# Performance work log

Hardware: AMD Instinct MI355X
Metric: run time of the kernel (lower is better)

Reference implementation:

```python
import jax, jax.numpy as jnp
import numpy as np

# structural constants (from dg config / init_kwargs)
B = 8192      # batch (L=1)
N = 64        # number of columns
C = 16        # one-hot width per column
D = N * C     # 1024
NUM = 32      # first NUM columns are numeric (use info['range'])
NCAUSAL = 16  # causal_cols = range(16)
K = 8         # info['range'][i] is [C, K]
HS = 1024
HP = 1024
TAU = 0.7
SMOOTH = 0.1  # kwargs['smoothing']


def setup_inputs() -> dict:
    key = jax.random.key(0)
    ks = jax.random.split(key, 20)
    s = 0.02
    inp = {
        'x': jax.random.uniform(ks[0], (B, D), dtype=jnp.float32),
        'truth_x': jax.random.normal(ks[1], (B, N), dtype=jnp.float32),
        # selector: Linear(D,HS) -> ReLU -> Linear(HS,N) -> Sigmoid
        'sel_w1': jax.random.normal(ks[2], (D, HS)) * s,
        'sel_b1': jnp.zeros((HS,), jnp.float32),
        'sel_w2': jax.random.normal(ks[3], (HS, N)) * s,
        'sel_b2': jnp.zeros((N,), jnp.float32),
        # perturber: D->HP->HP->HP->D with ReLU between
        'pw1': jax.random.normal(ks[4], (D, HP)) * s,
        'pb1': jnp.zeros((HP,), jnp.float32),
        'pw2': jax.random.normal(ks[5], (HP, HP)) * s,
        'pb2': jnp.zeros((HP,), jnp.float32),
        'pw3': jax.random.normal(ks[6], (HP, HP)) * s,
        'pb3': jnp.zeros((HP,), jnp.float32),
        'pw4': jax.random.normal(ks[7], (HP, D)) * s,
        'pb4': jnp.zeros((D,), jnp.float32),
        # dg.info['range'][i] for numeric columns: [NUM, C, K]
        'ranges': jax.random.normal(ks[8], (NUM, C, K), dtype=jnp.float32),
        # pre-drawn noise (training branch)
        'unif_a': jax.random.uniform(ks[9], (B, N), minval=1e-6, maxval=1.0 - 1e-6),
        'unif_b': jax.random.uniform(ks[10], (B, N), minval=1e-6, maxval=1.0 - 1e-6),
        'gumbel': jax.random.gumbel(ks[11], (B, N, C), dtype=jnp.float32),
    }
    return inp


def reference(x, truth_x, sel_w1, sel_b1, sel_w2, sel_b2,
              pw1, pb1, pw2, pb2, pw3, pb3, pw4, pb4,
              ranges, unif_a, unif_b, gumbel):
    # selector -> P in (0,1), shape [B, N]
    P = jax.nn.sigmoid(jax.nn.relu(x @ sel_w1 + sel_b1) @ sel_w2 + sel_b2)
    # relaxed Bernoulli (Sample_Bernoulli, training branch)
    ga = -jnp.log(-jnp.log(unif_a))
    gb = -jnp.log(-jnp.log(unif_b))
    no_logits = P * jnp.exp(ga) / TAU
    de_logits = no_logits + (1.0 - P) * jnp.exp(gb) / TAU
    probs = no_logits / de_logits                       # [B, N]
    # perturber MLP -> W, shape [B, D]
    h = jax.nn.relu(x @ pw1 + pb1)
    h = jax.nn.relu(h @ pw2 + pb2)
    h = jax.nn.relu(h @ pw3 + pb3)
    W = h @ pw4 + pb4
    # per-column blocks
    xr = x.reshape(B, N, C)
    logits = W.reshape(B, N, C)
    # data-dependent causal masking for causal columns
    curr = jnp.argmax(xr, axis=-1)                      # [B, N]
    causal = (jnp.arange(N) < NCAUSAL)[None, :, None]   # [1, N, 1]
    below = jnp.arange(C)[None, None, :] < curr[:, :, None]
    mask = jnp.where(causal & below, -100.0, jnp.where(causal, 1.0, 0.0))
    logits = logits + mask
    # label smoothing then Gumbel-softmax (soft), per Sample_Categorical
    pr = jax.nn.softmax(logits, axis=-1)
    pr = (1.0 - SMOOTH) * pr + SMOOTH / C
    logits = jnp.log(pr)
    y = jax.nn.softmax((logits + gumbel) / TAU, axis=-1)  # [B, N, C]
    # numeric columns: map categorical sample through range table, mix with truth
    xt_num = jnp.einsum('bnc,nck->bnk', y[:, :NUM], ranges).mean(axis=-1)  # [B, NUM]
    p_num = probs[:, :NUM]
    out_num = p_num * xt_num + (1.0 - p_num) * truth_x[:, :NUM]           # [B, NUM]
    # categorical columns: mix relaxed sample with original one-hot block
    p_cat = probs[:, NUM:, None]
    out_cat = p_cat * y[:, NUM:] + (1.0 - p_cat) * xr[:, NUM:]            # [B, N-NUM, C]
    xcf = jnp.concatenate([out_num, out_cat.reshape(B, (N - NUM) * C)], axis=1)
    return truth_x, xcf, P, W
```

## Files before the change

kernel.cpp:

```cpp
#include <hip/hip_runtime.h>
#include <hip/hip_bf16.h>
#include <cstdint>

#define B_DIM 8192
#define N_DIM 64
#define C_DIM 16
#define D_DIM 1024
#define NUM 32
#define NCAUSAL 16
#define K_RANGES 8
#define HS 1024
#define HP 1024
#define TAU 0.7f
#define SMOOTH 0.1f

typedef __bf16 bf16x8 __attribute__((ext_vector_type(8)));
typedef float f32x16 __attribute__((ext_vector_type(16)));

typedef const __attribute__((address_space(1))) uint32_t* gas_ptr;
typedef __attribute__((address_space(3))) uint32_t* las_ptr;

__device__ __forceinline__ void gld_lds16(const void* g, void* l) {
    __builtin_amdgcn_global_load_lds((gas_ptr)(uintptr_t)g,
                                     (las_ptr)(uint32_t)(uintptr_t)l,
                                     16, 0, 0);
}

__device__ __forceinline__ int swz(int r) { return (r & 3) ^ ((r >> 2) & 3); }

template <int ACT>
__device__ __forceinline__ void gemm_body8(
    const ushort* __restrict__ Ag, const ushort* __restrict__ Bg,
    const float* __restrict__ bias,
    float* __restrict__ Cf, __hip_bfloat16* __restrict__ Cb,
    int lda, int Nout, int ldC, int K, long m0, long n0,
    uint4 (*As)[512], uint4 (*Bs)[512])
{
    const int tid  = threadIdx.x;
    const int wave = tid >> 6;
    const int ln31 = tid & 31, blk = (tid >> 5) & 1;
    const int wr = wave >> 2, wc = wave & 3;

    const int row = tid >> 2;
    const int ch  = (tid & 3) ^ swz(row);
    const ushort* aSrc = Ag + (m0 + row) * (long)lda + ch * 8;
    const ushort* bSrc = Bg + (n0 + row) * (long)K   + ch * 8;
    const int ldsOff = wave << 6;

    f32x16 acc[2];
    acc[0] = (f32x16)(0.0f);
    acc[1] = (f32x16)(0.0f);

#define ISSUE_STAGE8(buf, kt)                                                  \
    {                                                                          \
        gld_lds16(aSrc + (kt), &As[buf][ldsOff]);                              \
        gld_lds16(bSrc + (kt), &Bs[buf][ldsOff]);                              \
    }

    const int nt = K >> 5;
    ISSUE_STAGE8(0, 0);
    ISSUE_STAGE8(1, 32);

    int rb = 0;
    for (int t = 0; t < nt; ++t) {
        if (t < nt - 1) {
            asm volatile("s_waitcnt vmcnt(2)" ::: "memory");
        } else {
            asm volatile("s_waitcnt vmcnt(0)" ::: "memory");
        }
        __builtin_amdgcn_s_barrier();

        if (t + 2 < nt) {
            int sb = rb + 2; if (sb >= 3) sb -= 3;
            ISSUE_STAGE8(sb, (t + 2) * 32);
        }

        bf16x8 af[2][2], bfr[2];
#pragma unroll
        for (int ks = 0; ks < 2; ++ks) {
            int c = ks * 2 + blk;
#pragma unroll
            for (int mi = 0; mi < 2; ++mi) {
                int r = wr * 64 + mi * 32 + ln31;
                af[ks][mi] = __builtin_bit_cast(bf16x8, As[rb][r * 4 + (c ^ swz(r))]);
            }
            int n = wc * 32 + ln31;
            bfr[ks] = __builtin_bit_cast(bf16x8, Bs[rb][n * 4 + (c ^ swz(n))]);
        }
#pragma unroll
        for (int ks = 0; ks < 2; ++ks)
#pragma unroll
            for (int mi = 0; mi < 2; ++mi)
                acc[mi] = __builtin_amdgcn_mfma_f32_32x32x16_bf16(
                    af[ks][mi], bfr[ks], acc[mi], 0, 0, 0);

        rb = (rb == 2) ? 0 : rb + 1;
    }
#undef ISSUE_STAGE8

    long col = n0 + wc * 32 + ln31;
    if (col < Nout) {
        float bs = bias ? bias[col] : 0.0f;
#pragma unroll
        for (int mi = 0; mi < 2; ++mi) {
#pragma unroll
            for (int reg = 0; reg < 16; ++reg) {
                long r2 = m0 + wr * 64 + mi * 32 + (reg & 3) + 8 * (reg >> 2) + 4 * blk;
                float v = acc[mi][reg] + bs;
                if (ACT == 1) {
                    v = fmaxf(v, 0.0f);
                    Cb[r2 * (long)ldC + col] = __float2bfloat16(v);
                } else if (ACT == 2) {
                    v = 1.0f / (1.0f + __expf(-v));
                    Cf[r2 * (long)ldC + col] = v;
                } else {
                    Cf[r2 * (long)ldC + col] = v;
                }
            }
        }
    }
}

__device__ __forceinline__ void xcd_remap(int& bx, int& by)
{
    int gx  = gridDim.x;
    int nwg = gx * gridDim.y;
    int lin = by * gx + bx;
    int cpx = nwg >> 3;
    int sw  = (lin & 7) * cpx + (lin >> 3);
    by = sw / gx;
    bx = sw - by * gx;
}

template <int ACT>
__global__ __launch_bounds__(512, 4) void gemm8(
    const __hip_bfloat16* __restrict__ A, const __hip_bfloat16* __restrict__ Bt,
    const float* __restrict__ bias,
    float* __restrict__ Cf, __hip_bfloat16* __restrict__ Cb,
    int lda, int Nout, int ldC, int K)
{
    __shared__ uint4 As[3][512];
    __shared__ uint4 Bs[3][512];
    int bx = blockIdx.x, by = blockIdx.y;
    xcd_remap(bx, by);
    gemm_body8<ACT>((const ushort*)A, (const ushort*)Bt, bias, Cf, Cb,
                    lda, Nout, ldC, K,
                    (long)by * 128, (long)bx * 128, As, Bs);
}

__global__ __launch_bounds__(512, 4) void gemm8_fused23(
    const __hip_bfloat16* __restrict__ act1,
    const __hip_bfloat16* __restrict__ p2t, const float* __restrict__ pb2,
    __hip_bfloat16* __restrict__ actB,
    const __hip_bfloat16* __restrict__ w2t, const float* __restrict__ sel_b2,
    float* __restrict__ outP)
{
    __shared__ uint4 As[3][512];
    __shared__ uint4 Bs[3][512];
    int bx = blockIdx.x, by = blockIdx.y;
    xcd_remap(bx, by);
    long m0 = (long)by * 128;
    if (bx < 8) {
        gemm_body8<1>((const ushort*)(act1 + 1024), (const ushort*)p2t, pb2,
                      nullptr, actB, 2048, 1024, 1024, 1024,
                      m0, (long)bx * 128, As, Bs);
    } else {
        gemm_body8<2>((const ushort*)act1, (const ushort*)w2t, sel_b2,
                      outP, nullptr, 2048, 64, 64, 1024,
                      m0, 0, As, Bs);
    }
}

struct PrepArgs {
    const float* src[6];
    __hip_bfloat16* dst[6];
    int Nsrc[6];
    int Npad[6];
    const float* ranges; float* rmean;
    const float* b1; const float* b2; float* bcat;
    const float* x; __hip_bfloat16* xbf;
};

__global__ void prep_kernel(PrepArgs a)
{
    int z = blockIdx.z;
    int tx = threadIdx.x, ty = threadIdx.y;
    int t = ty * 32 + tx;
    if (z == 7) {
        int bid = blockIdx.y * 32 + blockIdx.x;
        const float4* s4 = (const float4*)a.x;
        for (int i = bid * 256 + t; i < B_DIM * D_DIM / 4; i += 1024 * 256) {
            float4 v = s4[i];
            __hip_bfloat16* d = a.xbf + (size_t)i * 4;
            d[0] = __float2bfloat16(v.x);
            d[1] = __float2bfloat16(v.y);
            d[2] = __float2bfloat16(v.z);
            d[3] = __float2bfloat16(v.w);
        }
        return;
    }
    if (z == 6) {
        if (blockIdx.x || blockIdx.y) return;
        for (int j = t; j < NUM * C_DIM; j += 256) {
            float s = 0.0f;
#pragma unroll
            for (int k = 0; k < K_RANGES; ++k) s += a.ranges[j * K_RANGES + k];
            a.rmean[j] = s * (1.0f / K_RANGES);
        }
        for (int j = t; j < 1024; j += 256) {
            a.bcat[j]        = a.b1[j];
            a.bcat[1024 + j] = a.b2[j];
        }
        return;
    }
    const int Nsrc = a.Nsrc[z], Npad = a.Npad[z];
    int n0 = blockIdx.x * 32, k0 = blockIdx.y * 32;
    if (n0 >= Npad) return;
    const float* src = a.src[z];
    __hip_bfloat16* dst = a.dst[z];
    __shared__ float tile[32][33];
#pragma unroll
    for (int i = 0; i < 32; i += 8) {
        int k = k0 + ty + i, n = n0 + tx;
        tile[ty + i][tx] = (n < Nsrc) ? src[(size_t)k * Nsrc + n] : 0.0f;
    }
    __syncthreads();
#pragma unroll
    for (int i = 0; i < 32; i += 8) {
        int n = n0 + ty + i, k = k0 + tx;
        dst[(size_t)n * D_DIM + k] = __float2bfloat16(tile[tx][ty + i]);
    }
}

__global__ void finalize_kernel(
    const float* __restrict__ x, const float* __restrict__ truth,
    const float* __restrict__ ua, const float* __restrict__ ub,
    const float* __restrict__ gum, const float* __restrict__ rmean,
    const float* __restrict__ P, const float* __restrict__ W,
    float* __restrict__ out_truth, float* __restrict__ out_xcf)
{
    int idx = blockIdx.x * 256 + threadIdx.x;
    if (idx >= B_DIM * N_DIM) return;
    int b = idx >> 6, n = idx & 63;

    float tx = truth[idx];
    out_truth[idx] = tx;

    float p  = P[idx];
    float ea = -1.0f / logf(ua[idx]);
    float eb = -1.0f / logf(ub[idx]);
    float no = p * ea;
    float probs = no / (no + (1.0f - p) * eb);

    const float* Wrow = W + (size_t)idx * 16;
    const float* grow = gum + (size_t)idx * 16;
    float lo[16], g[16], xv[16];
#pragma unroll
    for (int c = 0; c < 16; c += 4) {
        float4 v = *(const float4*)(Wrow + c);
        lo[c] = v.x; lo[c + 1] = v.y; lo[c + 2] = v.z; lo[c + 3] = v.w;
        float4 gv = *(const float4*)(grow + c);
        g[c] = gv.x; g[c + 1] = gv.y; g[c + 2] = gv.z; g[c + 3] = gv.w;
    }

    bool needx = (n < NCAUSAL) || (n >= NUM);
    if (needx) {
        const float* xrow = x + (size_t)idx * 16;
#pragma unroll
        for (int c = 0; c < 16; c += 4) {
            float4 v = *(const float4*)(xrow + c);
            xv[c] = v.x; xv[c + 1] = v.y; xv[c + 2] = v.z; xv[c + 3] = v.w;
        }
    }

    if (n < NCAUSAL) {
        int curr = 0; float best = xv[0];
#pragma unroll
        for (int c = 1; c < 16; ++c)
            if (xv[c] > best) { best = xv[c]; curr = c; }
#pragma unroll
        for (int c = 0; c < 16; ++c) lo[c] += (c < curr) ? -100.0f : 1.0f;
    }

    float mx = lo[0];
#pragma unroll
    for (int c = 1; c < 16; ++c) mx = fmaxf(mx, lo[c]);
    float s = 0.0f, pr[16];
#pragma unroll
    for (int c = 0; c < 16; ++c) { pr[c] = __expf(lo[c] - mx); s += pr[c]; }
    float inv = 1.0f / s;
#pragma unroll
    for (int c = 0; c < 16; ++c)
        pr[c] = (1.0f - SMOOTH) * pr[c] * inv + (SMOOTH / C_DIM);

    float t[16];
    float mx2 = -1e30f;
#pragma unroll
    for (int c = 0; c < 16; ++c) {
        t[c] = (__logf(pr[c]) + g[c]) * (1.0f / TAU);
        mx2 = fmaxf(mx2, t[c]);
    }
    float s2 = 0.0f;
#pragma unroll
    for (int c = 0; c < 16; ++c) { t[c] = __expf(t[c] - mx2); s2 += t[c]; }
    float inv2 = 1.0f / s2;

    if (n < NUM) {
        float xt = 0.0f;
#pragma unroll
        for (int c = 0; c < 16; ++c) xt += t[c] * inv2 * rmean[n * 16 + c];
        out_xcf[(size_t)b * 544 + n] = probs * xt + (1.0f - probs) * tx;
    } else {
        float* o = out_xcf + (size_t)b * 544 + 32 + (size_t)(n - NUM) * 16;
#pragma unroll
        for (int c = 0; c < 16; ++c)
            o[c] = probs * t[c] * inv2 + (1.0f - probs) * xv[c];
    }
}

extern "C" void kernel_launch(void* const* d_in, const int* in_sizes, int n_in,
                              void* d_out, int out_size, void* d_ws, size_t ws_size,
                              hipStream_t stream)
{
    const float* x      = (const float*)d_in[0];
    const float* truth  = (const float*)d_in[1];
    const float* sel_w1 = (const float*)d_in[2];
    const float* sel_b1 = (const float*)d_in[3];
    const float* sel_w2 = (const float*)d_in[4];
    const float* sel_b2 = (const float*)d_in[5];
    const float* pw1    = (const float*)d_in[6];
    const float* pb1    = (const float*)d_in[7];
    const float* pw2    = (const float*)d_in[8];
    const float* pb2    = (const float*)d_in[9];
    const float* pw3    = (const float*)d_in[10];
    const float* pb3    = (const float*)d_in[11];
    const float* pw4    = (const float*)d_in[12];
    const float* pb4    = (const float*)d_in[13];
    const float* ranges = (const float*)d_in[14];
    const float* ua     = (const float*)d_in[15];
    const float* ub     = (const float*)d_in[16];
    const float* gum    = (const float*)d_in[17];

    float* out       = (float*)d_out;
    float* out_truth = out;
    float* out_xcf   = out + 524288;
    float* out_P     = out + 4980736;
    float* out_W     = out + 5505024;

    char* w = (char*)d_ws;
    size_t off = 0;
    __hip_bfloat16* A0   = (__hip_bfloat16*)(w + off); off += (size_t)B_DIM * D_DIM * 2;
    __hip_bfloat16* act1 = (__hip_bfloat16*)(w + off); off += (size_t)B_DIM * 2048 * 2;
    __hip_bfloat16* actB = (__hip_bfloat16*)(w + off); off += (size_t)B_DIM * HP * 2;
    __hip_bfloat16* actC = (__hip_bfloat16*)(w + off); off += (size_t)B_DIM * HP * 2;
    __hip_bfloat16* Wcat = (__hip_bfloat16*)(w + off); off += (size_t)2048 * D_DIM * 2;
    __hip_bfloat16* w2t  = (__hip_bfloat16*)(w + off); off += (size_t)128 * HS * 2;
    __hip_bfloat16* p2t  = (__hip_bfloat16*)(w + off); off += (size_t)HP * HP * 2;
    __hip_bfloat16* p3t  = (__hip_bfloat16*)(w + off); off += (size_t)HP * HP * 2;
    __hip_bfloat16* p4t  = (__hip_bfloat16*)(w + off); off += (size_t)D_DIM * HP * 2;
    float* rmean         = (float*)(w + off);          off += 512 * 4;
    float* bcat          = (float*)(w + off);          off += 2048 * 4;
    if (ws_size < off) return;

    PrepArgs pa;
    pa.src[0] = sel_w1; pa.dst[0] = Wcat;               pa.Nsrc[0] = HS;    pa.Npad[0] = 1024;
    pa.src[1] = pw1;    pa.dst[1] = Wcat + 1024 * 1024; pa.Nsrc[1] = HP;    pa.Npad[1] = 1024;
    pa.src[2] = sel_w2; pa.dst[2] = w2t;                pa.Nsrc[2] = N_DIM; pa.Npad[2] = 128;
    pa.src[3] = pw2;    pa.dst[3] = p2t;                pa.Nsrc[3] = HP;    pa.Npad[3] = 1024;
    pa.src[4] = pw3;    pa.dst[4] = p3t;                pa.Nsrc[4] = HP;    pa.Npad[4] = 1024;
    pa.src[5] = pw4;    pa.dst[5] = p4t;                pa.Nsrc[5] = D_DIM; pa.Npad[5] = 1024;
    pa.ranges = ranges; pa.rmean = rmean;
    pa.b1 = sel_b1; pa.b2 = pb1; pa.bcat = bcat;
    pa.x = x; pa.xbf = A0;

    prep_kernel<<<dim3(32, 32, 8), dim3(32, 8), 0, stream>>>(pa);

    gemm8<1><<<dim3(16, 64), 512, 0, stream>>>(A0, Wcat, bcat, nullptr, act1,
                                               D_DIM, 2048, 2048, D_DIM);
    gemm8_fused23<<<dim3(9, 64), 512, 0, stream>>>(act1, p2t, pb2, actB, w2t,
                                                   sel_b2, out_P);
    gemm8<1><<<dim3(8, 64), 512, 0, stream>>>(actB, p3t, pb3, nullptr, actC,
                                              HP, HP, HP, HP);
    gemm8<0><<<dim3(8, 64), 512, 0, stream>>>(actC, p4t, pb4, out_W, nullptr,
                                              HP, D_DIM, D_DIM, HP);

    finalize_kernel<<<(B_DIM * N_DIM + 255) / 256, 256, 0, stream>>>(
        x, truth, ua, ub, gum, rmean, out_P, out_W, out_truth, out_xcf);
}
```

Before: 293.7 us.

## Restructure bf16 GEMMs into intra-block split-K with LDS reduction

Replaces the 3-stage pipelined GEMM body with a split-K design. Each of two wave groups handles half of a 64-wide K slice with a 64x64 per-wave sub-tile, and the partial accumulators are reduced through LDS before the bias/activation epilogue. The goal is more reuse of register fragments per MFMA (2x2 outputs per wave instead of 2x1) and fewer barriers per K. The cost is double buffering instead of triple, an extra LDS reduction pass, and higher register use (4 accumulators) that may hurt occupancy under launch_bounds(512,4).

Result: slower. 309.3 us (+5.3%).

```diff
diff --git a/kernel.cpp b/kernel.cpp
--- a/kernel.cpp
+++ b/kernel.cpp
@@ -28,99 +28,6 @@
 
 __device__ __forceinline__ int swz(int r) { return (r & 3) ^ ((r >> 2) & 3); }
 
-template <int ACT>
-__device__ __forceinline__ void gemm_body8(
-    const ushort* __restrict__ Ag, const ushort* __restrict__ Bg,
-    const float* __restrict__ bias,
-    float* __restrict__ Cf, __hip_bfloat16* __restrict__ Cb,
-    int lda, int Nout, int ldC, int K, long m0, long n0,
-    uint4 (*As)[512], uint4 (*Bs)[512])
-{
-    const int tid  = threadIdx.x;
-    const int wave = tid >> 6;
-    const int ln31 = tid & 31, blk = (tid >> 5) & 1;
-    const int wr = wave >> 2, wc = wave & 3;
-
-    const int row = tid >> 2;
-    const int ch  = (tid & 3) ^ swz(row);
-    const ushort* aSrc = Ag + (m0 + row) * (long)lda + ch * 8;
-    const ushort* bSrc = Bg + (n0 + row) * (long)K   + ch * 8;
-    const int ldsOff = wave << 6;
-
-    f32x16 acc[2];
-    acc[0] = (f32x16)(0.0f);
-    acc[1] = (f32x16)(0.0f);
-
-#define ISSUE_STAGE8(buf, kt)                                                  \
-    {                                                                          \
-        gld_lds16(aSrc + (kt), &As[buf][ldsOff]);                              \
-        gld_lds16(bSrc + (kt), &Bs[buf][ldsOff]);                              \
-    }
-
-    const int nt = K >> 5;
-    ISSUE_STAGE8(0, 0);
-    ISSUE_STAGE8(1, 32);
-
-    int rb = 0;
-    for (int t = 0; t < nt; ++t) {
-        if (t < nt - 1) {
-            asm volatile("s_waitcnt vmcnt(2)" ::: "memory");
-        } else {
-            asm volatile("s_waitcnt vmcnt(0)" ::: "memory");
-        }
-        __builtin_amdgcn_s_barrier();
-
-        if (t + 2 < nt) {
-            int sb = rb + 2; if (sb >= 3) sb -= 3;
-            ISSUE_STAGE8(sb, (t + 2) * 32);
-        }
-
-        bf16x8 af[2][2], bfr[2];
-#pragma unroll
-        for (int ks = 0; ks < 2; ++ks) {
-            int c = ks * 2 + blk;
-#pragma unroll
-            for (int mi = 0; mi < 2; ++mi) {
-                int r = wr * 64 + mi * 32 + ln31;
-                af[ks][mi] = __builtin_bit_cast(bf16x8, As[rb][r * 4 + (c ^ swz(r))]);
-            }
-            int n = wc * 32 + ln31;
-            bfr[ks] = __builtin_bit_cast(bf16x8, Bs[rb][n * 4 + (c ^ swz(n))]);
-        }
-#pragma unroll
-        for (int ks = 0; ks < 2; ++ks)
-#pragma unroll
-            for (int mi = 0; mi < 2; ++mi)
-                acc[mi] = __builtin_amdgcn_mfma_f32_32x32x16_bf16(
-                    af[ks][mi], bfr[ks], acc[mi], 0, 0, 0);
-
-        rb = (rb == 2) ? 0 : rb + 1;
-    }
-#undef ISSUE_STAGE8
-
-    long col = n0 + wc * 32 + ln31;
-    if (col < Nout) {
-        float bs = bias ? bias[col] : 0.0f;
-#pragma unroll
-        for (int mi = 0; mi < 2; ++mi) {
-#pragma unroll
-            for (int reg = 0; reg < 16; ++reg) {
-                long r2 = m0 + wr * 64 + mi * 32 + (reg & 3) + 8 * (reg >> 2) + 4 * blk;
-                float v = acc[mi][reg] + bs;
-                if (ACT == 1) {
-                    v = fmaxf(v, 0.0f);
-                    Cb[r2 * (long)ldC + col] = __float2bfloat16(v);
-                } else if (ACT == 2) {
-                    v = 1.0f / (1.0f + __expf(-v));
-                    Cf[r2 * (long)ldC + col] = v;
-                } else {
-                    Cf[r2 * (long)ldC + col] = v;
-                }
-            }
-        }
-    }
-}
-
 __device__ __forceinline__ void xcd_remap(int& bx, int& by)
 {
     int gx  = gridDim.x;
@@ -133,41 +40,168 @@
 }
 
 template <int ACT>
-__global__ __launch_bounds__(512, 4) void gemm8(
+__device__ __forceinline__ void gemm_ks_body(
+    const ushort* __restrict__ Ag, const ushort* __restrict__ Bg,
+    const float* __restrict__ bias,
+    float* __restrict__ Cf, __hip_bfloat16* __restrict__ Cb,
+    int lda, int Nout, int ldC, int K, long m0, long n0,
+    uint4* lds)
+{
+    const int tid  = threadIdx.x;
+    const int wave = tid >> 6;
+    const int lane = tid & 63;
+    const int ln31 = tid & 31, blk = (tid >> 5) & 1;
+    const int wr = (wave >> 1) & 1, wc = wave & 1, kg = wave >> 2;
+
+    const int row = tid >> 2;
+    const int ch  = (tid & 3) ^ swz(row);
+    const ushort* aSrc = Ag + (m0 + row) * (long)lda + ch * 8;
+    const ushort* bSrc = Bg + (n0 + row) * (long)K   + ch * 8;
+    const int ldsOff = wave << 6;
+
+    f32x16 acc[2][2];
+#pragma unroll
+    for (int i = 0; i < 2; ++i)
+#pragma unroll
+        for (int j = 0; j < 2; ++j) acc[i][j] = (f32x16)(0.0f);
+
+#define STG(buf, kt)                                                           \
+    {                                                                          \
+        gld_lds16(aSrc + (kt),      &lds[(buf) * 1024 + ldsOff]);              \
+        gld_lds16(aSrc + (kt) + 32, &lds[(buf) * 1024 + 512 + ldsOff]);        \
+        gld_lds16(bSrc + (kt),      &lds[2048 + (buf) * 1024 + ldsOff]);       \
+        gld_lds16(bSrc + (kt) + 32, &lds[2048 + (buf) * 1024 + 512 + ldsOff]); \
+    }
+
+    STG(0, 0);
+    int cur = 0;
+    for (int kt = 0; kt < K; kt += 64) {
+        __syncthreads();
+        if (kt + 64 < K) STG(cur ^ 1, kt + 64);
+
+        const uint4* Ar = lds + cur * 1024 + kg * 512;
+        const uint4* Br = lds + 2048 + cur * 1024 + kg * 512;
+
+        bf16x8 af[2][2], bfr[2][2];
+#pragma unroll
+        for (int ks = 0; ks < 2; ++ks) {
+            int c = ks * 2 + blk;
+#pragma unroll
+            for (int mi = 0; mi < 2; ++mi) {
+                int r = wr * 64 + mi * 32 + ln31;
+                af[ks][mi] = __builtin_bit_cast(bf16x8, Ar[r * 4 + (c ^ swz(r))]);
+            }
+#pragma unroll
+            for (int ni = 0; ni < 2; ++ni) {
+                int n = wc * 64 + ni * 32 + ln31;
+                bfr[ks][ni] = __builtin_bit_cast(bf16x8, Br[n * 4 + (c ^ swz(n))]);
+            }
+        }
+#pragma unroll
+        for (int ks = 0; ks < 2; ++ks)
+#pragma unroll
+            for (int mi = 0; mi < 2; ++mi)
+#pragma unroll
+                for (int ni = 0; ni < 2; ++ni)
+                    acc[mi][ni] = __builtin_amdgcn_mfma_f32_32x32x16_bf16(
+                        af[ks][mi], bfr[ks][ni], acc[mi][ni], 0, 0, 0);
+        cur ^= 1;
+    }
+#undef STG
+
+    __syncthreads();
+    const int rbase = (wr * 2 + wc) * 1024;
+    if (kg == 1) {
+#pragma unroll
+        for (int mi = 0; mi < 2; ++mi)
+#pragma unroll
+            for (int ni = 0; ni < 2; ++ni)
+#pragma unroll
+                for (int q = 0; q < 4; ++q) {
+                    float4 t = { acc[mi][ni][q * 4 + 0], acc[mi][ni][q * 4 + 1],
+                                 acc[mi][ni][q * 4 + 2], acc[mi][ni][q * 4 + 3] };
+                    int i = mi * 8 + ni * 4 + q;
+                    lds[rbase + lane * 16 + (i ^ (lane & 7))] =
+                        __builtin_bit_cast(uint4, t);
+                }
+    }
+    __syncthreads();
+    if (kg == 0) {
+#pragma unroll
+        for (int mi = 0; mi < 2; ++mi)
+#pragma unroll
+            for (int ni = 0; ni < 2; ++ni)
+#pragma unroll
+                for (int q = 0; q < 4; ++q) {
+                    int i = mi * 8 + ni * 4 + q;
+                    float4 t = __builtin_bit_cast(
+                        float4, lds[rbase + lane * 16 + (i ^ (lane & 7))]);
+                    acc[mi][ni][q * 4 + 0] += t.x;
+                    acc[mi][ni][q * 4 + 1] += t.y;
+                    acc[mi][ni][q * 4 + 2] += t.z;
+                    acc[mi][ni][q * 4 + 3] += t.w;
+                }
+
+#pragma unroll
+        for (int ni = 0; ni < 2; ++ni) {
+            long col = n0 + wc * 64 + ni * 32 + ln31;
+            if (col >= Nout) continue;
+            float bs = bias ? bias[col] : 0.0f;
+#pragma unroll
+            for (int mi = 0; mi < 2; ++mi) {
+#pragma unroll
+                for (int reg = 0; reg < 16; ++reg) {
+                    long r2 = m0 + wr * 64 + mi * 32 + (reg & 3) + 8 * (reg >> 2) + 4 * blk;
+                    float v = acc[mi][ni][reg] + bs;
+                    if (ACT == 1) {
+                        v = fmaxf(v, 0.0f);
+                        Cb[r2 * (long)ldC + col] = __float2bfloat16(v);
+                    } else if (ACT == 2) {
+                        v = 1.0f / (1.0f + __expf(-v));
+                        Cf[r2 * (long)ldC + col] = v;
+                    } else {
+                        Cf[r2 * (long)ldC + col] = v;
+                    }
+                }
+            }
+        }
+    }
+}
+
+template <int ACT>
+__global__ __launch_bounds__(512, 4) void gemm_ks(
     const __hip_bfloat16* __restrict__ A, const __hip_bfloat16* __restrict__ Bt,
     const float* __restrict__ bias,
     float* __restrict__ Cf, __hip_bfloat16* __restrict__ Cb,
     int lda, int Nout, int ldC, int K)
 {
-    __shared__ uint4 As[3][512];
-    __shared__ uint4 Bs[3][512];
+    __shared__ uint4 lds[4096];
     int bx = blockIdx.x, by = blockIdx.y;
     xcd_remap(bx, by);
-    gemm_body8<ACT>((const ushort*)A, (const ushort*)Bt, bias, Cf, Cb,
-                    lda, Nout, ldC, K,
-                    (long)by * 128, (long)bx * 128, As, Bs);
-}
-
-__global__ __launch_bounds__(512, 4) void gemm8_fused23(
+    gemm_ks_body<ACT>((const ushort*)A, (const ushort*)Bt, bias, Cf, Cb,
+                      lda, Nout, ldC, K,
+                      (long)by * 128, (long)bx * 128, lds);
+}
+
+__global__ __launch_bounds__(512, 4) void gemm_ks_fused23(
     const __hip_bfloat16* __restrict__ act1,
     const __hip_bfloat16* __restrict__ p2t, const float* __restrict__ pb2,
     __hip_bfloat16* __restrict__ actB,
     const __hip_bfloat16* __restrict__ w2t, const float* __restrict__ sel_b2,
     float* __restrict__ outP)
 {
-    __shared__ uint4 As[3][512];
-    __shared__ uint4 Bs[3][512];
+    __shared__ uint4 lds[4096];
     int bx = blockIdx.x, by = blockIdx.y;
     xcd_remap(bx, by);
     long m0 = (long)by * 128;
     if (bx < 8) {
-        gemm_body8<1>((const ushort*)(act1 + 1024), (const ushort*)p2t, pb2,
-                      nullptr, actB, 2048, 1024, 1024, 1024,
-                      m0, (long)bx * 128, As, Bs);
+        gemm_ks_body<1>((const ushort*)(act1 + 1024), (const ushort*)p2t, pb2,
+                        nullptr, actB, 2048, 1024, 1024, 1024,
+                        m0, (long)bx * 128, lds);
     } else {
-        gemm_body8<2>((const ushort*)act1, (const ushort*)w2t, sel_b2,
-                      outP, nullptr, 2048, 64, 64, 1024,
-                      m0, 0, As, Bs);
+        gemm_ks_body<2>((const ushort*)act1, (const ushort*)w2t, sel_b2,
+                        outP, nullptr, 2048, 64, 64, 1024,
+                        m0, 0, lds);
     }
 }
 
@@ -375,14 +409,14 @@
 
     prep_kernel<<<dim3(32, 32, 8), dim3(32, 8), 0, stream>>>(pa);
 
-    gemm8<1><<<dim3(16, 64), 512, 0, stream>>>(A0, Wcat, bcat, nullptr, act1,
-                                               D_DIM, 2048, 2048, D_DIM);
-    gemm8_fused23<<<dim3(9, 64), 512, 0, stream>>>(act1, p2t, pb2, actB, w2t,
-                                                   sel_b2, out_P);
-    gemm8<1><<<dim3(8, 64), 512, 0, stream>>>(actB, p3t, pb3, nullptr, actC,
-                                              HP, HP, HP, HP);
-    gemm8<0><<<dim3(8, 64), 512, 0, stream>>>(actC, p4t, pb4, out_W, nullptr,
-                                              HP, D_DIM, D_DIM, HP);
+    gemm_ks<1><<<dim3(16, 64), 512, 0, stream>>>(A0, Wcat, bcat, nullptr, act1,
+                                                 D_DIM, 2048, 2048, D_DIM);
+    gemm_ks_fused23<<<dim3(9, 64), 512, 0, stream>>>(act1, p2t, pb2, actB, w2t,
+                                                     sel_b2, out_P);
+    gemm_ks<1><<<dim3(8, 64), 512, 0, stream>>>(actB, p3t, pb3, nullptr, actC,
+                                                HP, HP, HP, HP);
+    gemm_ks<0><<<dim3(8, 64), 512, 0, stream>>>(actC, p4t, pb4, out_W, nullptr,
+                                                HP, D_DIM, D_DIM, HP);
 
     finalize_kernel<<<(B_DIM * N_DIM + 255) / 256, 256, 0, stream>>>(
         x, truth, ua, ub, gum, rmean, out_P, out_W, out_truth, out_xcf);
```

## Fuse MLP layers and finalize into one persistent cooperative kernel

Applied to the files above, without the earlier changes.

Runs all GEMM layers in a single cooperative-launched persistent kernel separated by grid-wide syncs, and fuses the finalize Gumbel-softmax step into the last GEMM epilogue by staging its accumulator tile in shared memory. This removes per-kernel launch gaps and the global re-read of W in finalize. It adds grid barrier costs and a fixed 512-block schedule that may load-balance worse, e.g. the selector head runs on only 64 blocks after layer 2; the old launch path is kept as a fallback.

New measurement: 782.3 us. 2.66x slower.

```diff
diff --git a/kernel.cpp b/kernel.cpp
--- a/kernel.cpp
+++ b/kernel.cpp
@@ -1,6 +1,9 @@
 #include <hip/hip_runtime.h>
 #include <hip/hip_bf16.h>
+#include <hip/hip_cooperative_groups.h>
 #include <cstdint>
+
+namespace cg = cooperative_groups;
 
 #define B_DIM 8192
 #define N_DIM 64
@@ -34,7 +37,7 @@
     const float* __restrict__ bias,
     float* __restrict__ Cf, __hip_bfloat16* __restrict__ Cb,
     int lda, int Nout, int ldC, int K, long m0, long n0,
-    uint4 (*As)[512], uint4 (*Bs)[512])
+    uint4 (*As)[512], uint4 (*Bs)[512], f32x16* accExp = nullptr)
 {
     const int tid  = threadIdx.x;
     const int wave = tid >> 6;
@@ -97,6 +100,8 @@
         rb = (rb == 2) ? 0 : rb + 1;
     }
 #undef ISSUE_STAGE8
+
+    if (ACT == 3) { accExp[0] = acc[0]; accExp[1] = acc[1]; }
 
     long col = n0 + wc * 32 + ln31;
     if (col < Nout) {
@@ -121,15 +126,179 @@
     }
 }
 
-__device__ __forceinline__ void xcd_remap(int& bx, int& by)
-{
-    int gx  = gridDim.x;
-    int nwg = gx * gridDim.y;
-    int lin = by * gx + bx;
-    int cpx = nwg >> 3;
-    int sw  = (lin & 7) * cpx + (lin >> 3);
-    by = sw / gx;
-    bx = sw - by * gx;
+struct NetArgs {
+    const ushort* A0; const ushort* Wcat; const float* bcat;
+    __hip_bfloat16* act1;
+    const ushort* p2t; const float* pb2; __hip_bfloat16* actB;
+    const ushort* w2t; const float* sel_b2; float* outP;
+    const ushort* p3t; const float* pb3; __hip_bfloat16* actC;
+    const ushort* p4t; const float* pb4; float* outW;
+    const float* x; const float* truth; const float* ua; const float* ub;
+    const float* gum; const float* rmean;
+    float* out_truth; float* out_xcf;
+};
+
+__global__ __launch_bounds__(512, 4) void net_kernel(NetArgs a)
+{
+    __shared__ uint4 smem[3072];
+    uint4 (*As)[512] = reinterpret_cast<uint4(*)[512]>(smem);
+    uint4 (*Bs)[512] = reinterpret_cast<uint4(*)[512]>(smem + 1536);
+
+    cg::grid_group grid = cg::this_grid();
+    const int b = blockIdx.x;
+
+#pragma unroll
+    for (int r = 0; r < 2; ++r) {
+        int lin = b + r * 512;
+        int sw  = (lin & 7) * 128 + (lin >> 3);
+        long m0 = (long)(sw >> 4) * 128;
+        long n0 = (long)(sw & 15) * 128;
+        gemm_body8<1>(a.A0, a.Wcat, a.bcat, nullptr, a.act1,
+                      1024, 2048, 2048, 1024, m0, n0, As, Bs);
+        __syncthreads();
+    }
+    __threadfence();
+    grid.sync();
+
+    {
+        int sw  = (b & 7) * 64 + (b >> 3);
+        long m0 = (long)(sw >> 3) * 128;
+        long n0 = (long)(sw & 7) * 128;
+        gemm_body8<1>((const ushort*)a.act1 + 1024, a.p2t, a.pb2,
+                      nullptr, a.actB, 2048, 1024, 1024, 1024, m0, n0, As, Bs);
+        __syncthreads();
+    }
+    if (b < 64) {
+        gemm_body8<2>((const ushort*)a.act1, a.w2t, a.sel_b2, a.outP, nullptr,
+                      2048, 64, 64, 1024, (long)b * 128, 0, As, Bs);
+        __syncthreads();
+    }
+    __threadfence();
+    grid.sync();
+
+    {
+        int sw  = (b & 7) * 64 + (b >> 3);
+        long m0 = (long)(sw >> 3) * 128;
+        long n0 = (long)(sw & 7) * 128;
+        gemm_body8<1>((const ushort*)a.actB, a.p3t, a.pb3, nullptr, a.actC,
+                      1024, 1024, 1024, 1024, m0, n0, As, Bs);
+        __syncthreads();
+    }
+    __threadfence();
+    grid.sync();
+
+    {
+        int sw  = (b & 7) * 64 + (b >> 3);
+        long m0 = (long)(sw >> 3) * 128;
+        long n0 = (long)(sw & 7) * 128;
+
+        f32x16 accE[2];
+        gemm_body8<3>((const ushort*)a.actC, a.p4t, a.pb4, a.outW, nullptr,
+                      1024, 1024, 1024, 1024, m0, n0, As, Bs, accE);
+
+        const int tid  = threadIdx.x;
+        const int wave = tid >> 6;
+        const int ln31 = tid & 31, blk2 = (tid >> 5) & 1;
+        const int wr = wave >> 2, wc = wave & 3;
+
+        float* tile = (float*)smem;
+        const float bs = a.pb4[n0 + wc * 32 + ln31];
+
+        const int lb = tid >> 3;
+        const int ng = tid & 7;
+        const int n  = (int)(n0 >> 4) + ng;
+
+        for (int h = 0; h < 2; ++h) {
+            __syncthreads();
+            if (wr == h) {
+#pragma unroll
+                for (int mi = 0; mi < 2; ++mi)
+#pragma unroll
+                    for (int reg = 0; reg < 16; ++reg) {
+                        int lr = mi * 32 + (reg & 3) + 8 * (reg >> 2) + 4 * blk2;
+                        tile[lr * 132 + wc * 32 + ln31] = accE[mi][reg] + bs;
+                    }
+            }
+            __syncthreads();
+
+            long bb  = m0 + h * 64 + lb;
+            long idx = bb * 64 + n;
+
+            float tx = a.truth[idx];
+            a.out_truth[idx] = tx;
+
+            float p  = a.outP[idx];
+            float ea = -1.0f / logf(a.ua[idx]);
+            float eb = -1.0f / logf(a.ub[idx]);
+            float no = p * ea;
+            float probs = no / (no + (1.0f - p) * eb);
+
+            const float* Wrow = tile + lb * 132 + ng * 16;
+            const float* grow = a.gum + (size_t)idx * 16;
+            float lo[16], g[16], xv[16];
+#pragma unroll
+            for (int c = 0; c < 16; c += 4) {
+                float4 v = *(const float4*)(Wrow + c);
+                lo[c] = v.x; lo[c + 1] = v.y; lo[c + 2] = v.z; lo[c + 3] = v.w;
+                float4 gv = *(const float4*)(grow + c);
+                g[c] = gv.x; g[c + 1] = gv.y; g[c + 2] = gv.z; g[c + 3] = gv.w;
+            }
+
+            bool needx = (n < NCAUSAL) || (n >= NUM);
+            if (needx) {
+                const float* xrow = a.x + (size_t)idx * 16;
+#pragma unroll
+                for (int c = 0; c < 16; c += 4) {
+                    float4 v = *(const float4*)(xrow + c);
+                    xv[c] = v.x; xv[c + 1] = v.y; xv[c + 2] = v.z; xv[c + 3] = v.w;
+                }
+            }
+
+            if (n < NCAUSAL) {
+                int curr = 0; float best = xv[0];
+#pragma unroll
+                for (int c = 1; c < 16; ++c)
+                    if (xv[c] > best) { best = xv[c]; curr = c; }
+#pragma unroll
+                for (int c = 0; c < 16; ++c) lo[c] += (c < curr) ? -100.0f : 1.0f;
+            }
+
+            float mx = lo[0];
+#pragma unroll
+            for (int c = 1; c < 16; ++c) mx = fmaxf(mx, lo[c]);
+            float s = 0.0f, pr[16];
+#pragma unroll
+            for (int c = 0; c < 16; ++c) { pr[c] = __expf(lo[c] - mx); s += pr[c]; }
+            float inv = 1.0f / s;
+#pragma unroll
+            for (int c = 0; c < 16; ++c)
+                pr[c] = (1.0f - SMOOTH) * pr[c] * inv + (SMOOTH / C_DIM);
+
+            float t[16];
+            float mx2 = -1e30f;
+#pragma unroll
+            for (int c = 0; c < 16; ++c) {
+                t[c] = (__logf(pr[c]) + g[c]) * (1.0f / TAU);
+                mx2 = fmaxf(mx2, t[c]);
+            }
+            float s2 = 0.0f;
+#pragma unroll
+            for (int c = 0; c < 16; ++c) { t[c] = __expf(t[c] - mx2); s2 += t[c]; }
+            float inv2 = 1.0f / s2;
+
+            if (n < NUM) {
+                float xt = 0.0f;
+#pragma unroll
+                for (int c = 0; c < 16; ++c) xt += t[c] * inv2 * a.rmean[n * 16 + c];
+                a.out_xcf[(size_t)bb * 544 + n] = probs * xt + (1.0f - probs) * tx;
+            } else {
+                float* o = a.out_xcf + (size_t)bb * 544 + 32 + (size_t)(n - NUM) * 16;
+#pragma unroll
+                for (int c = 0; c < 16; ++c)
+                    o[c] = probs * t[c] * inv2 + (1.0f - probs) * xv[c];
+            }
+        }
+    }
 }
 
 template <int ACT>
@@ -141,11 +310,12 @@
 {
     __shared__ uint4 As[3][512];
     __shared__ uint4 Bs[3][512];
-    int bx = blockIdx.x, by = blockIdx.y;
-    xcd_remap(bx, by);
+    int gx = gridDim.x, nwg = gx * gridDim.y;
+    int lin = blockIdx.y * gx + blockIdx.x;
+    int sw = (lin & 7) * (nwg >> 3) + (lin >> 3);
+    int by = sw / gx, bx = sw - by * gx;
     gemm_body8<ACT>((const ushort*)A, (const ushort*)Bt, bias, Cf, Cb,
-                    lda, Nout, ldC, K,
-                    (long)by * 128, (long)bx * 128, As, Bs);
+                    lda, Nout, ldC, K, (long)by * 128, (long)bx * 128, As, Bs);
 }
 
 __global__ __launch_bounds__(512, 4) void gemm8_fused23(
@@ -157,8 +327,10 @@
 {
     __shared__ uint4 As[3][512];
     __shared__ uint4 Bs[3][512];
-    int bx = blockIdx.x, by = blockIdx.y;
-    xcd_remap(bx, by);
+    int gx = gridDim.x, nwg = gx * gridDim.y;
+    int lin = blockIdx.y * gx + blockIdx.x;
+    int sw = (lin & 7) * (nwg >> 3) + (lin >> 3);
+    int by = sw / gx, bx = sw - by * gx;
     long m0 = (long)by * 128;
     if (bx < 8) {
         gemm_body8<1>((const ushort*)(act1 + 1024), (const ushort*)p2t, pb2,
@@ -166,8 +338,88 @@
                       m0, (long)bx * 128, As, Bs);
     } else {
         gemm_body8<2>((const ushort*)act1, (const ushort*)w2t, sel_b2,
-                      outP, nullptr, 2048, 64, 64, 1024,
-                      m0, 0, As, Bs);
+                      outP, nullptr, 2048, 64, 64, 1024, m0, 0, As, Bs);
+    }
+}
+
+__global__ void finalize_kernel(
+    const float* __restrict__ x, const float* __restrict__ truth,
+    const float* __restrict__ ua, const float* __restrict__ ub,
+    const float* __restrict__ gum, const float* __restrict__ rmean,
+    const float* __restrict__ P, const float* __restrict__ W,
+    float* __restrict__ out_truth, float* __restrict__ out_xcf)
+{
+    int idx = blockIdx.x * 256 + threadIdx.x;
+    if (idx >= B_DIM * N_DIM) return;
+    int b = idx >> 6, n = idx & 63;
+
+    float tx = truth[idx];
+    out_truth[idx] = tx;
+
+    float p  = P[idx];
+    float ea = -1.0f / logf(ua[idx]);
+    float eb = -1.0f / logf(ub[idx]);
+    float no = p * ea;
+    float probs = no / (no + (1.0f - p) * eb);
+
+    const float* Wrow = W + (size_t)idx * 16;
+    const float* grow = gum + (size_t)idx * 16;
+    float lo[16], g[16], xv[16];
+#pragma unroll
+    for (int c = 0; c < 16; c += 4) {
+        float4 v = *(const float4*)(Wrow + c);
+        lo[c] = v.x; lo[c + 1] = v.y; lo[c + 2] = v.z; lo[c + 3] = v.w;
+        float4 gv = *(const float4*)(grow + c);
+        g[c] = gv.x; g[c + 1] = gv.y; g[c + 2] = gv.z; g[c + 3] = gv.w;
+    }
+    bool needx = (n < NCAUSAL) || (n >= NUM);
+    if (needx) {
+        const float* xrow = x + (size_t)idx * 16;
+#pragma unroll
+        for (int c = 0; c < 16; c += 4) {
+            float4 v = *(const float4*)(xrow + c);
+            xv[c] = v.x; xv[c + 1] = v.y; xv[c + 2] = v.z; xv[c + 3] = v.w;
+        }
+    }
+    if (n < NCAUSAL) {
+        int curr = 0; float best = xv[0];
+#pragma unroll
+        for (int c = 1; c < 16; ++c)
+            if (xv[c] > best) { best = xv[c]; curr = c; }
+#pragma unroll
+        for (int c = 0; c < 16; ++c) lo[c] += (c < curr) ? -100.0f : 1.0f;
+    }
+    float mx = lo[0];
+#pragma unroll
+    for (int c = 1; c < 16; ++c) mx = fmaxf(mx, lo[c]);
+    float s = 0.0f, pr[16];
+#pragma unroll
+    for (int c = 0; c < 16; ++c) { pr[c] = __expf(lo[c] - mx); s += pr[c]; }
+    float inv = 1.0f / s;
+#pragma unroll
+    for (int c = 0; c < 16; ++c)
+        pr[c] = (1.0f - SMOOTH) * pr[c] * inv + (SMOOTH / C_DIM);
+    float t[16];
+    float mx2 = -1e30f;
+#pragma unroll
+    for (int c = 0; c < 16; ++c) {
+        t[c] = (__logf(pr[c]) + g[c]) * (1.0f / TAU);
+        mx2 = fmaxf(mx2, t[c]);
+    }
+    float s2 = 0.0f;
+#pragma unroll
+    for (int c = 0; c < 16; ++c) { t[c] = __expf(t[c] - mx2); s2 += t[c]; }
+    float inv2 = 1.0f / s2;
+    if (n < NUM) {
+        float xt = 0.0f;
+#pragma unroll
+        for (int c = 0; c < 16; ++c) xt += t[c] * inv2 * rmean[n * 16 + c];
+        out_xcf[(size_t)b * 544 + n] = probs * xt + (1.0f - probs) * tx;
+    } else {
+        float* o = out_xcf + (size_t)b * 544 + 32 + (size_t)(n - NUM) * 16;
+#pragma unroll
+        for (int c = 0; c < 16; ++c)
+            o[c] = probs * t[c] * inv2 + (1.0f - probs) * xv[c];
     }
 }
 
@@ -229,92 +481,6 @@
     for (int i = 0; i < 32; i += 8) {
         int n = n0 + ty + i, k = k0 + tx;
         dst[(size_t)n * D_DIM + k] = __float2bfloat16(tile[tx][ty + i]);
-    }
-}
-
-__global__ void finalize_kernel(
-    const float* __restrict__ x, const float* __restrict__ truth,
-    const float* __restrict__ ua, const float* __restrict__ ub,
-    const float* __restrict__ gum, const float* __restrict__ rmean,
-    const float* __restrict__ P, const float* __restrict__ W,
-    float* __restrict__ out_truth, float* __restrict__ out_xcf)
-{
-    int idx = blockIdx.x * 256 + threadIdx.x;
-    if (idx >= B_DIM * N_DIM) return;
-    int b = idx >> 6, n = idx & 63;
-
-    float tx = truth[idx];
-    out_truth[idx] = tx;
-
-    float p  = P[idx];
-    float ea = -1.0f / logf(ua[idx]);
-    float eb = -1.0f / logf(ub[idx]);
-    float no = p * ea;
-    float probs = no / (no + (1.0f - p) * eb);
-
-    const float* Wrow = W + (size_t)idx * 16;
-    const float* grow = gum + (size_t)idx * 16;
-    float lo[16], g[16], xv[16];
-#pragma unroll
-    for (int c = 0; c < 16; c += 4) {
-        float4 v = *(const float4*)(Wrow + c);
-        lo[c] = v.x; lo[c + 1] = v.y; lo[c + 2] = v.z; lo[c + 3] = v.w;
-        float4 gv = *(const float4*)(grow + c);
-        g[c] = gv.x; g[c + 1] = gv.y; g[c + 2] = gv.z; g[c + 3] = gv.w;
-    }
-
-    bool needx = (n < NCAUSAL) || (n >= NUM);
-    if (needx) {
-        const float* xrow = x + (size_t)idx * 16;
-#pragma unroll
-        for (int c = 0; c < 16; c += 4) {
-            float4 v = *(const float4*)(xrow + c);
-            xv[c] = v.x; xv[c + 1] = v.y; xv[c + 2] = v.z; xv[c + 3] = v.w;
-        }
-    }
-
-    if (n < NCAUSAL) {
-        int curr = 0; float best = xv[0];
-#pragma unroll
-        for (int c = 1; c < 16; ++c)
-            if (xv[c] > best) { best = xv[c]; curr = c; }
-#pragma unroll
-        for (int c = 0; c < 16; ++c) lo[c] += (c < curr) ? -100.0f : 1.0f;
-    }
-
-    float mx = lo[0];
-#pragma unroll
-    for (int c = 1; c < 16; ++c) mx = fmaxf(mx, lo[c]);
-    float s = 0.0f, pr[16];
-#pragma unroll
-    for (int c = 0; c < 16; ++c) { pr[c] = __expf(lo[c] - mx); s += pr[c]; }
-    float inv = 1.0f / s;
-#pragma unroll
-    for (int c = 0; c < 16; ++c)
-        pr[c] = (1.0f - SMOOTH) * pr[c] * inv + (SMOOTH / C_DIM);
-
-    float t[16];
-    float mx2 = -1e30f;
-#pragma unroll
-    for (int c = 0; c < 16; ++c) {
-        t[c] = (__logf(pr[c]) + g[c]) * (1.0f / TAU);
-        mx2 = fmaxf(mx2, t[c]);
-    }
-    float s2 = 0.0f;
-#pragma unroll
-    for (int c = 0; c < 16; ++c) { t[c] = __expf(t[c] - mx2); s2 += t[c]; }
-    float inv2 = 1.0f / s2;
-
-    if (n < NUM) {
-        float xt = 0.0f;
-#pragma unroll
-        for (int c = 0; c < 16; ++c) xt += t[c] * inv2 * rmean[n * 16 + c];
-        out_xcf[(size_t)b * 544 + n] = probs * xt + (1.0f - probs) * tx;
-    } else {
-        float* o = out_xcf + (size_t)b * 544 + 32 + (size_t)(n - NUM) * 16;
-#pragma unroll
-        for (int c = 0; c < 16; ++c)
-            o[c] = probs * t[c] * inv2 + (1.0f - probs) * xv[c];
     }
 }
 
@@ -375,6 +541,21 @@
 
     prep_kernel<<<dim3(32, 32, 8), dim3(32, 8), 0, stream>>>(pa);
 
+    NetArgs na;
+    na.A0 = (const ushort*)A0;   na.Wcat = (const ushort*)Wcat; na.bcat = bcat;
+    na.act1 = act1;
+    na.p2t = (const ushort*)p2t; na.pb2 = pb2; na.actB = actB;
+    na.w2t = (const ushort*)w2t; na.sel_b2 = sel_b2; na.outP = out_P;
+    na.p3t = (const ushort*)p3t; na.pb3 = pb3; na.actC = actC;
+    na.p4t = (const ushort*)p4t; na.pb4 = pb4; na.outW = out_W;
+    na.x = x; na.truth = truth; na.ua = ua; na.ub = ub; na.gum = gum;
+    na.rmean = rmean; na.out_truth = out_truth; na.out_xcf = out_xcf;
+
+    void* kargs[] = { &na };
+    hipError_t e = hipLaunchCooperativeKernel((const void*)net_kernel,
+                                              dim3(512), dim3(512), kargs, 0, stream);
+    if (e == hipSuccess) return;
+
     gemm8<1><<<dim3(16, 64), 512, 0, stream>>>(A0, Wcat, bcat, nullptr, act1,
                                                D_DIM, 2048, 2048, D_DIM);
     gemm8_fused23<<<dim3(9, 64), 512, 0, stream>>>(act1, p2t, pb2, actB, w2t,
@@ -383,7 +564,6 @@
                                               HP, HP, HP, HP);
     gemm8<0><<<dim3(8, 64), 512, 0, stream>>>(actC, p4t, pb4, out_W, nullptr,
                                               HP, D_DIM, D_DIM, HP);
-
     finalize_kernel<<<(B_DIM * N_DIM + 255) / 256, 256, 0, stream>>>(
         x, truth, ua, ub, gum, rmean, out_P, out_W, out_truth, out_xcf);
 }
```
